# Kernel optimization log

Measured on AMD Instinct MI355X. Metric: run time of the kernel, lower is better.

The kernel has to match this reference:

```python
import jax, jax.numpy as jnp
import numpy as np

N = 100000   # entities per side
E = 400000   # undirected edges per side
D = 256      # embedding dim
L = 2        # GCN layers
SEEDS = 10000
EPS = 1e-12  # torch F.normalize eps


def setup_inputs() -> dict:
    key = jax.random.key(0)
    ks = jax.random.split(key, 8)
    # xavier_uniform over the combined (2N, D) table, then split (as in __init__)
    scale = np.sqrt(6.0 / (2 * N + D)).astype(np.float32)
    feats_sr = jax.random.uniform(ks[0], (N, D), jnp.float32, -scale, scale)
    feats_tg = jax.random.uniform(ks[1], (N, D), jnp.float32, -scale, scale)
    edges_sr = jax.random.randint(ks[2], (E, 2), 0, N, dtype=jnp.int32)
    edges_tg = jax.random.randint(ks[3], (E, 2), 0, N, dtype=jnp.int32)
    sr_ent_seeds = jax.random.randint(ks[4], (SEEDS,), 0, N, dtype=jnp.int32)
    tg_ent_seeds = jax.random.randint(ks[5], (SEEDS,), 0, N, dtype=jnp.int32)
    triples_sr = jax.random.randint(ks[6], (E, 3), 0, N, dtype=jnp.int32)
    triples_tg = jax.random.randint(ks[7], (E, 3), 0, N, dtype=jnp.int32)
    return {"feats_sr": feats_sr, "feats_tg": feats_tg,
            "edges_sr": edges_sr, "edges_tg": edges_tg,
            "sr_ent_seeds": sr_ent_seeds, "tg_ent_seeds": tg_ent_seeds,
            "triples_sr": triples_sr, "triples_tg": triples_tg}


def gcn(edges, h):
    """layer_num stacked featureless GCN layers: h <- D^-1/2 (A+A^T+I) D^-1/2 h,
    ReLU between layers (not after last), no weight matrix / residual."""
    n = h.shape[0]
    loop = jnp.arange(n, dtype=edges.dtype)
    src = jnp.concatenate([edges[:, 0], edges[:, 1], loop])
    dst = jnp.concatenate([edges[:, 1], edges[:, 0], loop])
    deg = jax.ops.segment_sum(jnp.ones_like(dst, dtype=h.dtype), dst, num_segments=n)
    dinv = jax.lax.rsqrt(jnp.maximum(deg, 1.0))
    w = (dinv[src] * dinv[dst])[:, None]          # [E', 1] symmetric norm coeffs
    for i in range(L):
        msg = h[src] * w                          # gather + scale  [E', D]
        h = jax.ops.segment_sum(msg, dst, num_segments=n)  # scatter-add [N, D]
        if i < L - 1:
            h = jax.nn.relu(h)
    return h


def l2norm(h):
    return h / jnp.maximum(jnp.linalg.norm(h, axis=-1, keepdims=True), EPS)


def reference(feats_sr, feats_tg, edges_sr, edges_tg,
              sr_ent_seeds, tg_ent_seeds, triples_sr, triples_tg):
    sr_ent_hid = l2norm(gcn(edges_sr, feats_sr))
    tg_ent_hid = l2norm(gcn(edges_tg, feats_tg))
    sr_seed_hid = sr_ent_hid[sr_ent_seeds]
    tg_seed_hid = tg_ent_hid[tg_ent_seeds]
    return (sr_seed_hid, tg_seed_hid, sr_ent_hid, tg_ent_hid)
```

## Files before the change

### kernel.cpp

```cpp
#include <hip/hip_runtime.h>
#include <hip/hip_bf16.h>
#include <stdint.h>

#define N_ENT  100000
#define N_EDGE 400000
#define DIM    256
#define N_SEED 10000
#define SBLK   1024
#define NSB    98
#define RP_STRIDE (N_ENT + 64)

typedef unsigned short u16;

__device__ __forceinline__ float bf16_to_f(u16 u) {
    union { uint32_t i; float f; } v;
    v.i = ((uint32_t)u) << 16;
    return v.f;
}
__device__ __forceinline__ u16 f_to_bf16(float f) {
    union { uint32_t i; float f; } v; v.f = f;
    uint32_t x = v.i;
    return (u16)((x + 0x7FFFu + ((x >> 16) & 1u)) >> 16);
}

__global__ void detect_kernel(const void* feats, int* flag) {
    __shared__ int bad;
    if (threadIdx.x == 0) bad = 0;
    __syncthreads();
    const u16* p = (const u16*)feats;
    float v = fabsf(bf16_to_f(p[threadIdx.x]));
    if (!(v <= 0.01f)) atomicOr(&bad, 1);
    __syncthreads();
    if (threadIdx.x == 0) *flag = bad ? 0 : 1;
}

__global__ void degcnt2_kernel(const int* __restrict__ e_sr, const int* __restrict__ e_tg,
                               int* __restrict__ deg) {
    int e = blockIdx.x * blockDim.x + threadIdx.x;
    if (e >= N_EDGE) return;
    const int* ed = blockIdx.y ? e_tg : e_sr;
    int* dg = deg + blockIdx.y * N_ENT;
    atomicAdd(&dg[ed[2 * e]],     1);
    atomicAdd(&dg[ed[2 * e + 1]], 1);
}

__global__ void dinv2_kernel(const int* __restrict__ deg, float* __restrict__ dinv) {
    int i = blockIdx.x * blockDim.x + threadIdx.x;
    if (i < N_ENT) {
        int j = blockIdx.y * N_ENT + i;
        dinv[j] = rsqrtf((float)deg[j] + 1.0f);
    }
}

__global__ void scanA_kernel(const int* __restrict__ deg, int* __restrict__ bsum) {
    int side = blockIdx.y;
    const int* d = deg + side * N_ENT;
    int t = threadIdx.x;
    int base = blockIdx.x * SBLK + t * 4;
    int v0 = 0, v1 = 0, v2 = 0, v3 = 0;
    if (base + 3 < N_ENT) {
        int4 q = *(const int4*)(d + base);
        v0 = q.x; v1 = q.y; v2 = q.z; v3 = q.w;
    } else {
        if (base     < N_ENT) v0 = d[base];
        if (base + 1 < N_ENT) v1 = d[base + 1];
        if (base + 2 < N_ENT) v2 = d[base + 2];
    }
    int s = v0 + v1 + v2 + v3;
    #pragma unroll
    for (int o = 1; o < 64; o <<= 1) s += __shfl_xor(s, o, 64);
    __shared__ int lds[4];
    if ((t & 63) == 0) lds[t >> 6] = s;
    __syncthreads();
    if (t == 0) bsum[side * 128 + blockIdx.x] = lds[0] + lds[1] + lds[2] + lds[3];
}

__global__ void scanB_kernel(const int* __restrict__ bsum, int* __restrict__ boff,
                             int* __restrict__ rowptr) {
    int side = blockIdx.y;
    __shared__ int lds[128];
    int t = threadIdx.x;
    int v = (t < NSB) ? bsum[side * 128 + t] : 0;
    lds[t] = v;
    __syncthreads();
    for (int o = 1; o < 128; o <<= 1) {
        int u = (t >= o) ? lds[t - o] : 0;
        __syncthreads();
        lds[t] += u;
        __syncthreads();
    }
    if (t < NSB) boff[side * 128 + t] = lds[t] - v;
    if (t == 0)  rowptr[side * RP_STRIDE + N_ENT] = 2 * N_EDGE;
}

__global__ void scanC_kernel(const int* __restrict__ deg, const int* __restrict__ boff,
                             int* __restrict__ rowptr, int* __restrict__ cursor) {
    int side = blockIdx.y;
    const int* d = deg + side * N_ENT;
    int* rp = rowptr + side * RP_STRIDE;
    int* cu = cursor + side * N_ENT;
    int t = threadIdx.x;
    int lane = t & 63, wave = t >> 6;
    int base = blockIdx.x * SBLK + t * 4;
    int v0 = 0, v1 = 0, v2 = 0, v3 = 0;
    if (base + 3 < N_ENT) {
        int4 q = *(const int4*)(d + base);
        v0 = q.x; v1 = q.y; v2 = q.z; v3 = q.w;
    } else {
        if (base     < N_ENT) v0 = d[base];
        if (base + 1 < N_ENT) v1 = d[base + 1];
        if (base + 2 < N_ENT) v2 = d[base + 2];
    }
    int s = v0 + v1 + v2 + v3;
    int incl = s;
    #pragma unroll
    for (int o = 1; o < 64; o <<= 1) {
        int u = __shfl_up(incl, o, 64);
        if (lane >= o) incl += u;
    }
    int wexcl = incl - s;
    __shared__ int lds[4];
    if (lane == 63) lds[wave] = incl;
    __syncthreads();
    int wsum = 0;
    for (int w = 0; w < wave; ++w) wsum += lds[w];
    int off = boff[side * 128 + blockIdx.x] + wsum + wexcl;
    int e0 = off, e1 = off + v0, e2 = e1 + v1, e3 = e2 + v2;
    if (base     < N_ENT) { rp[base]     = e0; cu[base]     = e0; }
    if (base + 1 < N_ENT) { rp[base + 1] = e1; cu[base + 1] = e1; }
    if (base + 2 < N_ENT) { rp[base + 2] = e2; cu[base + 2] = e2; }
    if (base + 3 < N_ENT) { rp[base + 3] = e3; cu[base + 3] = e3; }
}

__global__ void fill2_kernel(const int* __restrict__ e_sr, const int* __restrict__ e_tg,
                             int* __restrict__ cursor, int* __restrict__ colx) {
    int e = blockIdx.x * blockDim.x + threadIdx.x;
    if (e >= N_EDGE) return;
    const int* ed = blockIdx.y ? e_tg : e_sr;
    int* cu = cursor + blockIdx.y * N_ENT;
    int* cx = colx   + blockIdx.y * (2 * N_EDGE);
    int a = ed[2 * e], b = ed[2 * e + 1];
    cx[atomicAdd(&cu[b], 1)] = a;
    cx[atomicAdd(&cu[a], 1)] = b;
}

__global__ void pull1_kernel(const void* __restrict__ feats, const int* __restrict__ rowptr,
                             const int* __restrict__ colx, const float* __restrict__ dinv,
                             float* __restrict__ h1, const int* __restrict__ flag) {
    int gw   = (blockIdx.x * blockDim.x + threadIdx.x) >> 6;
    if (gw >= N_ENT) return;
    int lane = threadIdx.x & 63, off = lane * 4;
    int d = gw;
    int k = rowptr[d], end = rowptr[d + 1];
    float dd = dinv[d];
    int use_bf = *flag;
    float a0, a1, a2, a3;
    {
        float w = dd * dd, x0, x1, x2, x3;
        if (use_bf) {
            ushort4 q = *(const ushort4*)((const u16*)feats + d * DIM + off);
            x0 = bf16_to_f(q.x); x1 = bf16_to_f(q.y); x2 = bf16_to_f(q.z); x3 = bf16_to_f(q.w);
        } else {
            float4 q = *(const float4*)((const float*)feats + d * DIM + off);
            x0 = q.x; x1 = q.y; x2 = q.z; x3 = q.w;
        }
        a0 = x0 * w; a1 = x1 * w; a2 = x2 * w; a3 = x3 * w;
    }
    if (k < end) {
        int c = colx[k];
        for (;;) {
            int cn = (k + 1 < end) ? colx[k + 1] : 0;
            float w = dinv[c] * dd, x0, x1, x2, x3;
            if (use_bf) {
                ushort4 q = *(const ushort4*)((const u16*)feats + c * DIM + off);
                x0 = bf16_to_f(q.x); x1 = bf16_to_f(q.y); x2 = bf16_to_f(q.z); x3 = bf16_to_f(q.w);
            } else {
                float4 q = *(const float4*)((const float*)feats + c * DIM + off);
                x0 = q.x; x1 = q.y; x2 = q.z; x3 = q.w;
            }
            a0 += x0 * w; a1 += x1 * w; a2 += x2 * w; a3 += x3 * w;
            if (++k >= end) break;
            c = cn;
        }
    }
    float4 o;
    o.x = fmaxf(a0, 0.0f); o.y = fmaxf(a1, 0.0f);
    o.z = fmaxf(a2, 0.0f); o.w = fmaxf(a3, 0.0f);
    *(float4*)(h1 + d * DIM + off) = o;
}

__global__ void pull2_kernel(const float* __restrict__ h1, const int* __restrict__ rowptr,
                             const int* __restrict__ colx, const float* __restrict__ dinv,
                             void* __restrict__ out, long long ent_off,
                             const int* __restrict__ flag) {
    int gw   = (blockIdx.x * blockDim.x + threadIdx.x) >> 6;
    if (gw >= N_ENT) return;
    int lane = threadIdx.x & 63, off = lane * 4;
    int d = gw;
    int k = rowptr[d], end = rowptr[d + 1];
    float dd = dinv[d];
    float w = dd * dd;
    float4 q = *(const float4*)(h1 + d * DIM + off);
    float a0 = q.x * w, a1 = q.y * w, a2 = q.z * w, a3 = q.w * w;
    if (k < end) {
        int c = colx[k];
        for (;;) {
            int cn = (k + 1 < end) ? colx[k + 1] : 0;
            float wc = dinv[c] * dd;
            float4 v = *(const float4*)(h1 + c * DIM + off);
            a0 += v.x * wc; a1 += v.y * wc; a2 += v.z * wc; a3 += v.w * wc;
            if (++k >= end) break;
            c = cn;
        }
    }
    float sq = a0 * a0 + a1 * a1 + a2 * a2 + a3 * a3;
    #pragma unroll
    for (int o = 1; o < 64; o <<= 1) sq += __shfl_xor(sq, o, 64);
    float inv = 1.0f / fmaxf(sqrtf(sq), 1e-12f);
    long long idx = ent_off + (long long)d * DIM + off;
    if (*flag) {
        ushort4 r;
        r.x = f_to_bf16(a0 * inv); r.y = f_to_bf16(a1 * inv);
        r.z = f_to_bf16(a2 * inv); r.w = f_to_bf16(a3 * inv);
        *(ushort4*)((u16*)out + idx) = r;
    } else {
        float4 r = { a0 * inv, a1 * inv, a2 * inv, a3 * inv };
        *(float4*)((float*)out + idx) = r;
    }
}

__global__ void seed_kernel(const int* __restrict__ seeds, void* __restrict__ out,
                            long long ent_off, long long seed_off, const int* __restrict__ flag) {
    int i = blockIdx.x;
    int t = threadIdx.x;
    int s = seeds[i];
    long long src = ent_off  + (long long)s * DIM + t;
    long long dst = seed_off + (long long)i * DIM + t;
    if (*flag) ((u16*)out)[dst]  = ((const u16*)out)[src];
    else       ((float*)out)[dst] = ((const float*)out)[src];
}

extern "C" void kernel_launch(void* const* d_in, const int* in_sizes, int n_in,
                              void* d_out, int out_size, void* d_ws, size_t ws_size,
                              hipStream_t stream) {
    const void* feats_sr = d_in[0];
    const void* feats_tg = d_in[1];
    const int*  edges_sr = (const int*)d_in[2];
    const int*  edges_tg = (const int*)d_in[3];
    const int*  sr_seeds = (const int*)d_in[4];
    const int*  tg_seeds = (const int*)d_in[5];

    char* ws = (char*)d_ws;
    int*   flag   = (int*)ws;
    int*   deg    = (int*)(ws + 256);
    float* dinv   = (float*)(ws + 800512);
    int*   rowptr = (int*)(ws + 1600768);
    int*   cursor = (int*)(ws + 2401280);
    int*   bsum   = (int*)(ws + 3201536);
    int*   boff   = (int*)(ws + 3202560);
    int*   colx   = (int*)(ws + 3203584);
    float* h1     = (float*)(ws + 9603840);

    detect_kernel<<<1, 256, 0, stream>>>(feats_sr, flag);

    hipMemsetAsync(deg, 0, (size_t)2 * N_ENT * 4, stream);

    dim3 eg((N_EDGE + 255) / 256, 2);
    dim3 ng((N_ENT + 255) / 256, 2);
    dim3 sg(NSB, 2);
    degcnt2_kernel<<<eg, 256, 0, stream>>>(edges_sr, edges_tg, deg);
    dinv2_kernel<<<ng, 256, 0, stream>>>(deg, dinv);
    scanA_kernel<<<sg, 256, 0, stream>>>(deg, bsum);
    scanB_kernel<<<dim3(1, 2), 128, 0, stream>>>(bsum, boff, rowptr);
    scanC_kernel<<<sg, 256, 0, stream>>>(deg, boff, rowptr, cursor);
    fill2_kernel<<<eg, 256, 0, stream>>>(edges_sr, edges_tg, cursor, colx);

    const int pull_blk = (N_ENT + 3) / 4;

    for (int side = 0; side < 2; ++side) {
        const void* feats = side ? feats_tg : feats_sr;
        const int*  seeds = side ? tg_seeds : sr_seeds;
        const int*  rp    = rowptr + side * RP_STRIDE;
        const int*  cx    = colx   + side * (2 * N_EDGE);
        const float* dv   = dinv   + side * N_ENT;
        long long seed_off = (long long)side * N_SEED * DIM;
        long long ent_off  = (long long)2 * N_SEED * DIM + (long long)side * N_ENT * DIM;

        pull1_kernel<<<pull_blk, 256, 0, stream>>>(feats, rp, cx, dv, h1, flag);
        pull2_kernel<<<pull_blk, 256, 0, stream>>>(h1, rp, cx, dv, d_out, ent_off, flag);
        seed_kernel<<<N_SEED, 256, 0, stream>>>(seeds, d_out, ent_off, seed_off, flag);
    }
}
```

Baseline: 1.071 ms.

## Store intermediate GCN layer in bf16, batch both sides per launch, unroll by two

The intermediate hidden layer h1 is now stored as bf16 rather than fp32, which halves the bytes written in layer one and gathered in layer two. The two graph sides are handled by a single launch each for pull1, pull2 and the seed copy through blockIdx.y, cutting launches from six to three and giving each grid more parallelism. The neighbour loops are unrolled by two so that two gathers are in flight at once. In exchange the layer-one activations lose precision before layer two, and h1 must now hold both sides at the same time.

Result: faster. 941.5 us (-12.1%).

```diff
diff --git a/kernel.cpp b/kernel.cpp
--- a/kernel.cpp
+++ b/kernel.cpp
@@ -144,74 +144,109 @@
     cx[atomicAdd(&cu[a], 1)] = b;
 }
 
-__global__ void pull1_kernel(const void* __restrict__ feats, const int* __restrict__ rowptr,
-                             const int* __restrict__ colx, const float* __restrict__ dinv,
-                             float* __restrict__ h1, const int* __restrict__ flag) {
+__global__ void pull1_kernel(const void* __restrict__ feats_sr, const void* __restrict__ feats_tg,
+                             const int* __restrict__ rowptr, const int* __restrict__ colx,
+                             const float* __restrict__ dinv, u16* __restrict__ h1,
+                             const int* __restrict__ flag) {
+    int side = blockIdx.y;
     int gw   = (blockIdx.x * blockDim.x + threadIdx.x) >> 6;
     if (gw >= N_ENT) return;
     int lane = threadIdx.x & 63, off = lane * 4;
+    const void*  feats = side ? feats_tg : feats_sr;
+    const int*   rp = rowptr + side * RP_STRIDE;
+    const int*   cx = colx   + side * (2 * N_EDGE);
+    const float* dv = dinv   + side * N_ENT;
+    u16*         h  = h1 + (size_t)side * N_ENT * DIM;
     int d = gw;
-    int k = rowptr[d], end = rowptr[d + 1];
-    float dd = dinv[d];
+    int k = rp[d], end = rp[d + 1];
+    float dd = dv[d];
     int use_bf = *flag;
     float a0, a1, a2, a3;
     {
-        float w = dd * dd, x0, x1, x2, x3;
+        float w = dd * dd;
         if (use_bf) {
             ushort4 q = *(const ushort4*)((const u16*)feats + d * DIM + off);
-            x0 = bf16_to_f(q.x); x1 = bf16_to_f(q.y); x2 = bf16_to_f(q.z); x3 = bf16_to_f(q.w);
+            a0 = bf16_to_f(q.x) * w; a1 = bf16_to_f(q.y) * w;
+            a2 = bf16_to_f(q.z) * w; a3 = bf16_to_f(q.w) * w;
         } else {
             float4 q = *(const float4*)((const float*)feats + d * DIM + off);
-            x0 = q.x; x1 = q.y; x2 = q.z; x3 = q.w;
+            a0 = q.x * w; a1 = q.y * w; a2 = q.z * w; a3 = q.w * w;
         }
-        a0 = x0 * w; a1 = x1 * w; a2 = x2 * w; a3 = x3 * w;
+    }
+    while (k + 2 <= end) {
+        int c0 = cx[k], c1 = cx[k + 1];
+        float w0 = dv[c0] * dd, w1 = dv[c1] * dd;
+        if (use_bf) {
+            ushort4 q0 = *(const ushort4*)((const u16*)feats + c0 * DIM + off);
+            ushort4 q1 = *(const ushort4*)((const u16*)feats + c1 * DIM + off);
+            a0 += bf16_to_f(q0.x) * w0 + bf16_to_f(q1.x) * w1;
+            a1 += bf16_to_f(q0.y) * w0 + bf16_to_f(q1.y) * w1;
+            a2 += bf16_to_f(q0.z) * w0 + bf16_to_f(q1.z) * w1;
+            a3 += bf16_to_f(q0.w) * w0 + bf16_to_f(q1.w) * w1;
+        } else {
+            float4 q0 = *(const float4*)((const float*)feats + c0 * DIM + off);
+            float4 q1 = *(const float4*)((const float*)feats + c1 * DIM + off);
+            a0 += q0.x * w0 + q1.x * w1;
+            a1 += q0.y * w0 + q1.y * w1;
+            a2 += q0.z * w0 + q1.z * w1;
+            a3 += q0.w * w0 + q1.w * w1;
+        }
+        k += 2;
     }
     if (k < end) {
-        int c = colx[k];
-        for (;;) {
-            int cn = (k + 1 < end) ? colx[k + 1] : 0;
-            float w = dinv[c] * dd, x0, x1, x2, x3;
-            if (use_bf) {
-                ushort4 q = *(const ushort4*)((const u16*)feats + c * DIM + off);
-                x0 = bf16_to_f(q.x); x1 = bf16_to_f(q.y); x2 = bf16_to_f(q.z); x3 = bf16_to_f(q.w);
-            } else {
-                float4 q = *(const float4*)((const float*)feats + c * DIM + off);
-                x0 = q.x; x1 = q.y; x2 = q.z; x3 = q.w;
-            }
-            a0 += x0 * w; a1 += x1 * w; a2 += x2 * w; a3 += x3 * w;
-            if (++k >= end) break;
-            c = cn;
+        int c = cx[k];
+        float w = dv[c] * dd;
+        if (use_bf) {
+            ushort4 q = *(const ushort4*)((const u16*)feats + c * DIM + off);
+            a0 += bf16_to_f(q.x) * w; a1 += bf16_to_f(q.y) * w;
+            a2 += bf16_to_f(q.z) * w; a3 += bf16_to_f(q.w) * w;
+        } else {
+            float4 q = *(const float4*)((const float*)feats + c * DIM + off);
+            a0 += q.x * w; a1 += q.y * w; a2 += q.z * w; a3 += q.w * w;
         }
     }
-    float4 o;
-    o.x = fmaxf(a0, 0.0f); o.y = fmaxf(a1, 0.0f);
-    o.z = fmaxf(a2, 0.0f); o.w = fmaxf(a3, 0.0f);
-    *(float4*)(h1 + d * DIM + off) = o;
-}
-
-__global__ void pull2_kernel(const float* __restrict__ h1, const int* __restrict__ rowptr,
+    ushort4 r;
+    r.x = f_to_bf16(fmaxf(a0, 0.0f)); r.y = f_to_bf16(fmaxf(a1, 0.0f));
+    r.z = f_to_bf16(fmaxf(a2, 0.0f)); r.w = f_to_bf16(fmaxf(a3, 0.0f));
+    *(ushort4*)(h + d * DIM + off) = r;
+}
+
+__global__ void pull2_kernel(const u16* __restrict__ h1, const int* __restrict__ rowptr,
                              const int* __restrict__ colx, const float* __restrict__ dinv,
-                             void* __restrict__ out, long long ent_off,
-                             const int* __restrict__ flag) {
+                             void* __restrict__ out, const int* __restrict__ flag) {
+    int side = blockIdx.y;
     int gw   = (blockIdx.x * blockDim.x + threadIdx.x) >> 6;
     if (gw >= N_ENT) return;
     int lane = threadIdx.x & 63, off = lane * 4;
+    const int*   rp = rowptr + side * RP_STRIDE;
+    const int*   cx = colx   + side * (2 * N_EDGE);
+    const float* dv = dinv   + side * N_ENT;
+    const u16*   h  = h1 + (size_t)side * N_ENT * DIM;
+    long long ent_off = (long long)2 * N_SEED * DIM + (long long)side * N_ENT * DIM;
     int d = gw;
-    int k = rowptr[d], end = rowptr[d + 1];
-    float dd = dinv[d];
+    int k = rp[d], end = rp[d + 1];
+    float dd = dv[d];
     float w = dd * dd;
-    float4 q = *(const float4*)(h1 + d * DIM + off);
-    float a0 = q.x * w, a1 = q.y * w, a2 = q.z * w, a3 = q.w * w;
+    ushort4 qs = *(const ushort4*)(h + d * DIM + off);
+    float a0 = bf16_to_f(qs.x) * w, a1 = bf16_to_f(qs.y) * w;
+    float a2 = bf16_to_f(qs.z) * w, a3 = bf16_to_f(qs.w) * w;
+    while (k + 2 <= end) {
+        int c0 = cx[k], c1 = cx[k + 1];
+        float w0 = dv[c0] * dd, w1 = dv[c1] * dd;
+        ushort4 q0 = *(const ushort4*)(h + c0 * DIM + off);
+        ushort4 q1 = *(const ushort4*)(h + c1 * DIM + off);
+        a0 += bf16_to_f(q0.x) * w0 + bf16_to_f(q1.x) * w1;
+        a1 += bf16_to_f(q0.y) * w0 + bf16_to_f(q1.y) * w1;
+        a2 += bf16_to_f(q0.z) * w0 + bf16_to_f(q1.z) * w1;
+        a3 += bf16_to_f(q0.w) * w0 + bf16_to_f(q1.w) * w1;
+        k += 2;
+    }
     if (k < end) {
-        int c = colx[k];
-        for (;;) {
-            int cn = (k + 1 < end) ? colx[k + 1] : 0;
-            float wc = dinv[c] * dd;
-            float4 v = *(const float4*)(h1 + c * DIM + off);
-            a0 += v.x * wc; a1 += v.y * wc; a2 += v.z * wc; a3 += v.w * wc;
-            if (++k >= end) break;
-            c = cn;
-        }
+        int c = cx[k];
+        float wc = dv[c] * dd;
+        ushort4 q = *(const ushort4*)(h + c * DIM + off);
+        a0 += bf16_to_f(q.x) * wc; a1 += bf16_to_f(q.y) * wc;
+        a2 += bf16_to_f(q.z) * wc; a3 += bf16_to_f(q.w) * wc;
     }
     float sq = a0 * a0 + a1 * a1 + a2 * a2 + a3 * a3;
     #pragma unroll
@@ -229,10 +264,14 @@
     }
 }
 
-__global__ void seed_kernel(const int* __restrict__ seeds, void* __restrict__ out,
-                            long long ent_off, long long seed_off, const int* __restrict__ flag) {
+__global__ void seed2_kernel(const int* __restrict__ s_sr, const int* __restrict__ s_tg,
+                             void* __restrict__ out, const int* __restrict__ flag) {
+    int side = blockIdx.y;
     int i = blockIdx.x;
     int t = threadIdx.x;
+    const int* seeds = side ? s_tg : s_sr;
+    long long ent_off  = (long long)2 * N_SEED * DIM + (long long)side * N_ENT * DIM;
+    long long seed_off = (long long)side * N_SEED * DIM;
     int s = seeds[i];
     long long src = ent_off  + (long long)s * DIM + t;
     long long dst = seed_off + (long long)i * DIM + t;
@@ -259,7 +298,7 @@
     int*   bsum   = (int*)(ws + 3201536);
     int*   boff   = (int*)(ws + 3202560);
     int*   colx   = (int*)(ws + 3203584);
-    float* h1     = (float*)(ws + 9603840);
+    u16*   h1     = (u16*)(ws + 9603840);
 
     detect_kernel<<<1, 256, 0, stream>>>(feats_sr, flag);
 
@@ -275,19 +314,8 @@
     scanC_kernel<<<sg, 256, 0, stream>>>(deg, boff, rowptr, cursor);
     fill2_kernel<<<eg, 256, 0, stream>>>(edges_sr, edges_tg, cursor, colx);
 
-    const int pull_blk = (N_ENT + 3) / 4;
-
-    for (int side = 0; side < 2; ++side) {
-        const void* feats = side ? feats_tg : feats_sr;
-        const int*  seeds = side ? tg_seeds : sr_seeds;
-        const int*  rp    = rowptr + side * RP_STRIDE;
-        const int*  cx    = colx   + side * (2 * N_EDGE);
-        const float* dv   = dinv   + side * N_ENT;
-        long long seed_off = (long long)side * N_SEED * DIM;
-        long long ent_off  = (long long)2 * N_SEED * DIM + (long long)side * N_ENT * DIM;
-
-        pull1_kernel<<<pull_blk, 256, 0, stream>>>(feats, rp, cx, dv, h1, flag);
-        pull2_kernel<<<pull_blk, 256, 0, stream>>>(h1, rp, cx, dv, d_out, ent_off, flag);
-        seed_kernel<<<N_SEED, 256, 0, stream>>>(seeds, d_out, ent_off, seed_off, flag);
-    }
-}
+    dim3 pg((N_ENT + 3) / 4, 2);
+    pull1_kernel<<<pg, 256, 0, stream>>>(feats_sr, feats_tg, rowptr, colx, dinv, h1, flag);
+    pull2_kernel<<<pg, 256, 0, stream>>>(h1, rowptr, colx, dinv, d_out, flag);
+    seed2_kernel<<<dim3(N_SEED, 2), 256, 0, stream>>>(sr_seeds, tg_seeds, d_out, flag);
+}
```
